# Kernel optimization log

Hardware: AMD Instinct MI355X
Metric: run time of the kernel (lower is better)

Reference implementation:

```python
import jax, jax.numpy as jnp
import numpy as np

NUM_HEADS = 8
EPS_OT = 0.05    # self.eps
BETA_T = 1.0     # self.beta_t
N_ITERS = 100    # Sinkhorn max_iter (reference runs all iterations; torch breaks early on convergence)


def setup_inputs() -> dict:
    key = jax.random.key(0)
    ks = jax.random.split(key, 10)
    B, N1, N2 = 16, 256, 576
    dim_t, dim_v, dim_out = 512, 512, 512
    s = 0.02  # conv1d k=1 init scale (stand-in for torch default init)
    f32 = jnp.float32
    return {
        "F_t": jax.random.normal(ks[0], (B, N1, dim_t), f32),
        "F_s": jax.random.normal(ks[1], (B, N2, dim_v), f32),
        # Conv1d(kernel_size=1) weights, squeezed to [out, in]; biases default-on in nn.Conv1d
        "Wq": jax.random.normal(ks[2], (dim_out, dim_t), f32) * s,
        "bq": jnp.zeros((dim_out,), f32),
        "Wk": jax.random.normal(ks[3], (dim_out, dim_v), f32) * s,
        "bk": jnp.zeros((dim_out,), f32),
        "Wv": jax.random.normal(ks[4], (dim_out, dim_v), f32) * s,
        "bv": jnp.zeros((dim_out,), f32),
        "Wp": jax.random.normal(ks[5], (dim_out, dim_out), f32) * s,
        "bp": jnp.zeros((dim_out,), f32),
    }


def sinkhorn_log_exp_sum(C, log_mu, log_nu, eps):
    # C: [BH, N1, N2]; fixed-length log-domain Sinkhorn.
    BH, N1, N2 = C.shape
    u0 = jnp.zeros((BH, N1), C.dtype)
    v0 = jnp.zeros((BH, N2), C.dtype)

    def body(carry, _):
        u, v = carry
        # single K per iteration; both u and v updates use the OLD (u, v), matching torch code
        K = (-C + u[:, :, None] + v[:, None, :]) / eps
        u_new = eps * (log_mu - jax.scipy.special.logsumexp(K, axis=2)) + u
        v_new = eps * (log_nu - jax.scipy.special.logsumexp(K, axis=1)) + v
        return (u_new, v_new), None

    (u, v), _ = jax.lax.scan(jax.checkpoint(body), (u0, v0), None, length=N_ITERS)
    return jnp.exp((-C + u[:, :, None] + v[:, None, :]) / eps)


def _l2norm(x, eps=1e-12):
    return x / jnp.maximum(jnp.linalg.norm(x, axis=-1, keepdims=True), eps)


def reference(F_t, F_s, Wq, bq, Wk, bk, Wv, bv, Wp, bp):
    B, N1, _ = F_t.shape
    N2 = F_s.shape[1]
    H = NUM_HEADS
    dim_out = Wq.shape[0]
    hd = dim_out // H

    # Conv1d(kernel=1) == pointwise linear over channel dim
    q = (F_t @ Wq.T + bq).reshape(B, N1, H, hd)
    k = (F_s @ Wk.T + bk).reshape(B, N2, H, hd)
    v = (F_s @ Wv.T + bv).reshape(B, N2, H, hd)

    q = _l2norm(q)
    k = _l2norm(k)

    sim = jnp.einsum('bnkc,bmkc->bknm', q, k) * BETA_T  # [B,H,N1,N2]
    wdist = (1.0 - sim).reshape(B * H, N1, N2)
    sim_f = sim.reshape(B * H, N1, N2)

    log_mu = jnp.log(jnp.asarray(1.0 / N1 + 1e-8, sim.dtype))
    log_nu = jnp.log(jnp.asarray(1.0 / N2 + 1e-8, sim.dtype))
    T = sinkhorn_log_exp_sum(wdist, log_mu, log_nu, EPS_OT)

    score_map = (N1 * N2 * sim_f * T).reshape(B, H, N1, N2)  # attn_drop = identity (p=0)
    F_t_a = jnp.einsum('bknm,bmkc->bnkc', score_map, v).reshape(B, N1, dim_out)
    F_t_a = F_t_a @ Wp.T + bp
    # torch: F_t_a / F_t_a.norm(dim=-1, keepdim=True)  (plain division, no eps clamp)
    F_t_a = F_t_a / jnp.linalg.norm(F_t_a, axis=-1, keepdims=True)
    return F_t_a  # proj_drop = identity (p=0)
```

## Files before the change

kernel.cpp:

```cpp
#include <hip/hip_runtime.h>
#include <math.h>

#define EPS_OT 0.05f
#define INV_EPS 20.0f

typedef unsigned short ushort_t;
typedef __attribute__((ext_vector_type(8))) short short8;
typedef __attribute__((ext_vector_type(4))) float f32x4;
union Pk { uint4 u; short8 s; };

__device__ __forceinline__ unsigned int f2bf(float f) {
  unsigned int u = __float_as_uint(f);
  return (u + 0x7FFFu + ((u >> 16) & 1u)) >> 16;
}
__device__ __forceinline__ float bf2f(unsigned int u) { return __uint_as_float(u << 16); }

__device__ __forceinline__ void bar_lds() {
  asm volatile("s_waitcnt lgkmcnt(0)" ::: "memory");
  __builtin_amdgcn_s_barrier();
  asm volatile("" ::: "memory");
}

__global__ __launch_bounds__(256) void pack_k(const float* __restrict__ F_t,
                                              const float* __restrict__ F_s,
                                              const float* __restrict__ Wq,
                                              const float* __restrict__ Wk,
                                              const float* __restrict__ Wv,
                                              const float* __restrict__ Wp,
                                              ushort_t* __restrict__ Fth, ushort_t* __restrict__ Ftl,
                                              ushort_t* __restrict__ Fsh, ushort_t* __restrict__ Fsl,
                                              ushort_t* __restrict__ Wqh, ushort_t* __restrict__ Wql,
                                              ushort_t* __restrict__ Wkh, ushort_t* __restrict__ Wkl,
                                              ushort_t* __restrict__ Wvh, ushort_t* __restrict__ Wvl,
                                              ushort_t* __restrict__ Wph) {
  const int blk = blockIdx.x;
  const float* src; ushort_t* dh; ushort_t* dl; size_t off;
  if (blk < 2048)      { src = F_t; dh = Fth; dl = Ftl; off = (size_t)blk * 1024; }
  else if (blk < 6656) { src = F_s; dh = Fsh; dl = Fsl; off = (size_t)(blk - 2048) * 1024; }
  else if (blk < 6912) { src = Wq;  dh = Wqh; dl = Wql; off = (size_t)(blk - 6656) * 1024; }
  else if (blk < 7168) { src = Wk;  dh = Wkh; dl = Wkl; off = (size_t)(blk - 6912) * 1024; }
  else if (blk < 7424) { src = Wv;  dh = Wvh; dl = Wvl; off = (size_t)(blk - 7168) * 1024; }
  else                 { src = Wp;  dh = Wph; dl = nullptr; off = (size_t)(blk - 7424) * 1024; }
  const size_t i = off + (size_t)threadIdx.x * 4;
  float4 f = *(const float4*)(src + i);
  unsigned int h0 = f2bf(f.x), h1 = f2bf(f.y), h2 = f2bf(f.z), h3 = f2bf(f.w);
  uint2 hh; hh.x = h0 | (h1 << 16); hh.y = h2 | (h3 << 16);
  *(uint2*)(dh + i) = hh;
  if (dl) {
    uint2 ll;
    ll.x = f2bf(f.x - bf2f(h0)) | (f2bf(f.y - bf2f(h1)) << 16);
    ll.y = f2bf(f.z - bf2f(h2)) | (f2bf(f.w - bf2f(h3)) << 16);
    *(uint2*)(dl + i) = ll;
  }
}

#define GEMM_HL_BODY()                                                                      \
  f32x4 acc[4] = {};                                                                        \
  for (int k0 = 0; k0 < 512; k0 += 64) {                                                    \
    uint4 a0 = *(const uint4*)(Xp_h + k0), a1 = *(const uint4*)(Xp_h + k0 + 8);             \
    uint4 b0 = *(const uint4*)(Xp_l + k0), b1 = *(const uint4*)(Xp_l + k0 + 8);             \
    uint4 c0 = *(const uint4*)(Wp_h + k0), c1 = *(const uint4*)(Wp_h + k0 + 8);             \
    uint4 d0 = *(const uint4*)(Wp_l + k0), d1 = *(const uint4*)(Wp_l + k0 + 8);             \
    __syncthreads();                                                                        \
    *(uint4*)&Xh[r][cg * 16] = a0; *(uint4*)&Xh[r][cg * 16 + 8] = a1;                       \
    *(uint4*)&Xl[r][cg * 16] = b0; *(uint4*)&Xl[r][cg * 16 + 8] = b1;                       \
    *(uint4*)&Wh[r][cg * 16] = c0; *(uint4*)&Wh[r][cg * 16 + 8] = c1;                       \
    *(uint4*)&Wl[r][cg * 16] = d0; *(uint4*)&Wl[r][cg * 16 + 8] = d1;                       \
    __syncthreads();                                                                        \
    _Pragma("unroll") for (int kst = 0; kst < 2; ++kst) {                                   \
      short8 ah = *(const short8*)&Xh[16 * w + li][kst * 32 + 8 * lg];                      \
      short8 al = *(const short8*)&Xl[16 * w + li][kst * 32 + 8 * lg];                      \
      _Pragma("unroll") for (int nt = 0; nt < 4; ++nt) {                                    \
        short8 bh = *(const short8*)&Wh[nt * 16 + li][kst * 32 + 8 * lg];                   \
        short8 bl = *(const short8*)&Wl[nt * 16 + li][kst * 32 + 8 * lg];                   \
        acc[nt] = __builtin_amdgcn_mfma_f32_16x16x32_bf16(ah, bh, acc[nt], 0, 0, 0);        \
        acc[nt] = __builtin_amdgcn_mfma_f32_16x16x32_bf16(ah, bl, acc[nt], 0, 0, 0);        \
        acc[nt] = __builtin_amdgcn_mfma_f32_16x16x32_bf16(al, bh, acc[nt], 0, 0, 0);        \
      }                                                                                     \
    }                                                                                       \
  }

#define GEMM_PL_BODY()                                                                      \
  f32x4 acc[4] = {};                                                                        \
  for (int k0 = 0; k0 < 512; k0 += 64) {                                                    \
    uint4 a0 = *(const uint4*)(Xp_h + k0), a1 = *(const uint4*)(Xp_h + k0 + 8);             \
    uint4 c0 = *(const uint4*)(Wp_h + k0), c1 = *(const uint4*)(Wp_h + k0 + 8);             \
    __syncthreads();                                                                        \
    *(uint4*)&Xh[r][cg * 16] = a0; *(uint4*)&Xh[r][cg * 16 + 8] = a1;                       \
    *(uint4*)&Wh[r][cg * 16] = c0; *(uint4*)&Wh[r][cg * 16 + 8] = c1;                       \
    __syncthreads();                                                                        \
    _Pragma("unroll") for (int kst = 0; kst < 2; ++kst) {                                   \
      short8 ah = *(const short8*)&Xh[16 * w + li][kst * 32 + 8 * lg];                      \
      _Pragma("unroll") for (int nt = 0; nt < 4; ++nt) {                                    \
        short8 bh = *(const short8*)&Wh[nt * 16 + li][kst * 32 + 8 * lg];                   \
        acc[nt] = __builtin_amdgcn_mfma_f32_16x16x32_bf16(ah, bh, acc[nt], 0, 0, 0);        \
      }                                                                                     \
    }                                                                                       \
  }

__global__ __launch_bounds__(256) void gemmnorm2_k(const ushort_t* __restrict__ Xg_h,
                                                   const ushort_t* __restrict__ Xg_l,
                                                   const ushort_t* __restrict__ Wg_h,
                                                   const ushort_t* __restrict__ Wg_l,
                                                   const float* __restrict__ bias,
                                                   ushort_t* __restrict__ oh,
                                                   ushort_t* __restrict__ ol, int Nn) {
  __shared__ ushort_t Xh[64][72], Xl[64][72], Wh[64][72], Wl[64][72];
  const int tid = threadIdx.x;
  const int w = tid >> 6, l = tid & 63, li = l & 15, lg = l >> 4;
  const int r = tid >> 2, cg = tid & 3;
  const int m0 = blockIdx.x << 6;
  const int h = blockIdx.y, n0 = h << 6;
  const ushort_t* Xp_h = Xg_h + (size_t)(m0 + r) * 512 + cg * 16;
  const ushort_t* Xp_l = Xg_l + (size_t)(m0 + r) * 512 + cg * 16;
  const ushort_t* Wp_h = Wg_h + (size_t)(n0 + r) * 512 + cg * 16;
  const ushort_t* Wp_l = Wg_l + (size_t)(n0 + r) * 512 + cg * 16;
  GEMM_HL_BODY()
  float v[4][4];
  float ss[4] = {0.f, 0.f, 0.f, 0.f};
#pragma unroll
  for (int nt = 0; nt < 4; ++nt) {
    float bb = bias[n0 + nt * 16 + li];
#pragma unroll
    for (int reg = 0; reg < 4; ++reg) {
      float y = acc[nt][reg] + bb;
      v[nt][reg] = y;
      ss[reg] = fmaf(y, y, ss[reg]);
    }
  }
#pragma unroll
  for (int off = 1; off < 16; off <<= 1)
#pragma unroll
    for (int reg = 0; reg < 4; ++reg) ss[reg] += __shfl_xor(ss[reg], off, 64);
  const int b = m0 / Nn;
  const int nbase = m0 - b * Nn;
  const size_t base = ((size_t)(b * 8 + h) * Nn + nbase + 16 * w + 4 * lg) * 64;
#pragma unroll
  for (int reg = 0; reg < 4; ++reg) {
    float inv = 1.0f / fmaxf(sqrtf(ss[reg]), 1e-12f);
#pragma unroll
    for (int nt = 0; nt < 4; ++nt) {
      float y = v[nt][reg] * inv;
      unsigned int hi = f2bf(y);
      size_t idx = base + (size_t)reg * 64 + nt * 16 + li;
      oh[idx] = (ushort_t)hi;
      ol[idx] = (ushort_t)f2bf(y - bf2f(hi));
    }
  }
}

__global__ __launch_bounds__(256) void gemmtrans2_k(const ushort_t* __restrict__ Xg_h,
                                                    const ushort_t* __restrict__ Wg_h,
                                                    const float* __restrict__ bias,
                                                    ushort_t* __restrict__ vt) {
  __shared__ ushort_t Xh[64][72], Wh[64][72];
  __shared__ ushort_t Vs[64 * 73];
  const int tid = threadIdx.x;
  const int w = tid >> 6, l = tid & 63, li = l & 15, lg = l >> 4;
  const int r = tid >> 2, cg = tid & 3;
  const int m0 = blockIdx.x << 6;
  const int h = blockIdx.y, n0 = h << 6;
  const ushort_t* Xp_h = Xg_h + (size_t)(m0 + r) * 512 + cg * 16;
  const ushort_t* Wp_h = Wg_h + (size_t)(n0 + r) * 512 + cg * 16;
  GEMM_PL_BODY()
#pragma unroll
  for (int nt = 0; nt < 4; ++nt) {
    float bb = bias[n0 + nt * 16 + li];
#pragma unroll
    for (int reg = 0; reg < 4; ++reg)
      Vs[(16 * w + 4 * lg + reg) * 73 + nt * 16 + li] = (ushort_t)f2bf(acc[nt][reg] + bb);
  }
  __syncthreads();
  const int a9 = m0 >> 6;
  const int b = a9 / 9;
  const int nbase = m0 - b * 576;
  const int s = b * 8 + h;
  const int c = tid >> 2, q4 = tid & 3;
  ushort_t tmp[16];
#pragma unroll
  for (int jj = 0; jj < 16; ++jj) tmp[jj] = Vs[(q4 * 16 + jj) * 73 + c];
  ushort_t* op = vt + ((size_t)s * 64 + c) * 576 + nbase + q4 * 16;
  *(uint4*)op = *(uint4*)&tmp[0];
  *(uint4*)(op + 8) = *(uint4*)&tmp[8];
}

__global__ __launch_bounds__(256) void gemmplain_k(const ushort_t* __restrict__ Xg_h,
                                                   const ushort_t* __restrict__ Wg_h,
                                                   const float* __restrict__ bias,
                                                   float* __restrict__ Y) {
  __shared__ ushort_t Xh[64][72], Wh[64][72];
  const int tid = threadIdx.x;
  const int w = tid >> 6, l = tid & 63, li = l & 15, lg = l >> 4;
  const int r = tid >> 2, cg = tid & 3;
  const int m0 = blockIdx.x << 6, n0 = blockIdx.y << 6;
  const ushort_t* Xp_h = Xg_h + (size_t)(m0 + r) * 512 + cg * 16;
  const ushort_t* Wp_h = Wg_h + (size_t)(n0 + r) * 512 + cg * 16;
  GEMM_PL_BODY()
#pragma unroll
  for (int nt = 0; nt < 4; ++nt) {
    float bb = bias[n0 + nt * 16 + li];
#pragma unroll
    for (int reg = 0; reg < 4; ++reg)
      Y[(size_t)(m0 + 16 * w + 4 * lg + reg) * 512 + n0 + nt * 16 + li] = acc[nt][reg] + bb;
  }
}

#define SK_SMEM 147456

__global__ __launch_bounds__(1024, 1) void sinkhorn17_k(const ushort_t* __restrict__ qh,
                                                        const ushort_t* __restrict__ ql,
                                                        const ushort_t* __restrict__ kh,
                                                        const ushort_t* __restrict__ kl,
                                                        ushort_t* __restrict__ Eo,
                                                        float* __restrict__ gA,
                                                        float* __restrict__ gB,
                                                        unsigned long long* __restrict__ gpart,
                                                        float C_mu, float C_nu) {
  extern __shared__ char smem[];
  const int g = blockIdx.x, s = g >> 1, rh = g & 1, pg = g ^ 1;
  const int tid = threadIdx.x, w = tid >> 6, l = tid & 63, li = l & 15, lg = l >> 4;
  unsigned long long* myP = gpart + (size_t)g * 1152;
  const unsigned long long* prP = gpart + (size_t)pg * 1152;

  ushort_t* Elds = (ushort_t*)smem;
  {
    const int rt = w & 7;
    const int qrow = rh * 128 + rt * 16 + li;
    const size_t qoff = ((size_t)s * 256 + qrow) * 64 + 8 * lg;
    short8 aH0 = *(const short8*)(qh + qoff), aH1 = *(const short8*)(qh + qoff + 32);
    short8 aL0 = *(const short8*)(ql + qoff), aL1 = *(const short8*)(ql + qoff + 32);
    const int c0 = (w >> 3) * 18;
    for (int ci = 0; ci < 18; ++ci) {
      const int ct = c0 + ci;
      const size_t koff = ((size_t)s * 576 + ct * 16 + li) * 64 + 8 * lg;
      short8 bH0 = *(const short8*)(kh + koff), bH1 = *(const short8*)(kh + koff + 32);
      short8 bL0 = *(const short8*)(kl + koff), bL1 = *(const short8*)(kl + koff + 32);
      f32x4 acc = {0.f, 0.f, 0.f, 0.f};
      acc = __builtin_amdgcn_mfma_f32_16x16x32_bf16(aH0, bH0, acc, 0, 0, 0);
      acc = __builtin_amdgcn_mfma_f32_16x16x32_bf16(aH1, bH1, acc, 0, 0, 0);
      acc = __builtin_amdgcn_mfma_f32_16x16x32_bf16(aH0, bL0, acc, 0, 0, 0);
      acc = __builtin_amdgcn_mfma_f32_16x16x32_bf16(aH1, bL1, acc, 0, 0, 0);
      acc = __builtin_amdgcn_mfma_f32_16x16x32_bf16(aL0, bH0, acc, 0, 0, 0);
      acc = __builtin_amdgcn_mfma_f32_16x16x32_bf16(aL1, bH1, acc, 0, 0, 0);
#pragma unroll
      for (int reg = 0; reg < 4; ++reg) {
        float e = __expf((acc[reg] - 1.0f) * INV_EPS);
        Elds[(rt * 16 + 4 * lg + reg) * 576 + ct * 16 + li] = (ushort_t)f2bf(e);
      }
    }
  }
  __syncthreads();
  {
    uint4* Eg4 = (uint4*)(Eo + (size_t)s * 147456 + (size_t)rh * 73728);
    const uint4* El4 = (const uint4*)Elds;
    for (int idx = tid; idx < 9216; idx += 1024) Eg4[idx] = El4[idx];
  }

  const int art = (w & 7) * 16 + li;
  const int akb = (w >> 3) * 9;
  short8 afr[9];
#pragma unroll
  for (int c = 0; c < 9; ++c)
    afr[c] = *(const short8*)(Elds + art * 576 + (akb + c) * 32 + 8 * lg);

  short8 bfr0, bfr1, bfr2, bfr3, bfr4, bfr5, bfr6, bfr7, bfr8, bfr9, bfr10, bfr11;
#define BFR_BUILD(dst, tc, q)                                                  \
  {                                                                            \
    const ushort_t* p = Elds + ((q) * 32 + 8 * lg) * 576 + (tc) * 16 + li;     \
    Pk pk;                                                                     \
    pk.u.x = (unsigned int)p[0]    | ((unsigned int)p[576]  << 16);            \
    pk.u.y = (unsigned int)p[1152] | ((unsigned int)p[1728] << 16);            \
    pk.u.z = (unsigned int)p[2304] | ((unsigned int)p[2880] << 16);            \
    pk.u.w = (unsigned int)p[3456] | ((unsigned int)p[4032] << 16);            \
    dst = pk.s;                                                                \
  }
  BFR_BUILD(bfr0, w, 0) BFR_BUILD(bfr1, w, 1) BFR_BUILD(bfr2, w, 2) BFR_BUILD(bfr3, w, 3)
  BFR_BUILD(bfr4, w + 16, 0) BFR_BUILD(bfr5, w + 16, 1)
  BFR_BUILD(bfr6, w + 16, 2) BFR_BUILD(bfr7, w + 16, 3)
  if (w < 4) {
    BFR_BUILD(bfr8, w + 32, 0) BFR_BUILD(bfr9, w + 32, 1)
    BFR_BUILD(bfr10, w + 32, 2) BFR_BUILD(bfr11, w + 32, 3)
  } else {
    bfr8 = bfr0; bfr9 = bfr1; bfr10 = bfr2; bfr11 = bfr3;
  }
  __syncthreads();

  float* uu = (float*)smem;
  float* vv = uu + 128;
  ushort_t* au = (ushort_t*)(vv + 576);
  ushort_t* bv = au + 128;
  float* rpart = (float*)(au + 768);
  float* cso = rpart + 256;

  if (tid < 128) { uu[tid] = 0.0f; au[tid] = (ushort_t)0x3F80; }
  if (tid < 576) { vv[tid] = 0.0f; bv[tid] = (ushort_t)0x3F80; }
  __syncthreads();

  const int jj = tid - 128;
  const bool poller = (tid >= 128) && (tid < 704);

  for (int t = 0; t < 100; ++t) {
    const int par = t & 1;
    {
      Pk q0, q1, q2, q3;
      q0.u = *(const uint4*)(au + 8 * lg);
      q1.u = *(const uint4*)(au + 32 + 8 * lg);
      q2.u = *(const uint4*)(au + 64 + 8 * lg);
      q3.u = *(const uint4*)(au + 96 + 8 * lg);
#define MV2_TILE(tc, f0, f1, f2, f3)                                                  \
      {                                                                               \
        f32x4 a2 = {0.f, 0.f, 0.f, 0.f}, b2 = {0.f, 0.f, 0.f, 0.f};                   \
        a2 = __builtin_amdgcn_mfma_f32_16x16x32_bf16(q0.s, f0, a2, 0, 0, 0);          \
        b2 = __builtin_amdgcn_mfma_f32_16x16x32_bf16(q2.s, f2, b2, 0, 0, 0);          \
        a2 = __builtin_amdgcn_mfma_f32_16x16x32_bf16(q1.s, f1, a2, 0, 0, 0);          \
        b2 = __builtin_amdgcn_mfma_f32_16x16x32_bf16(q3.s, f3, b2, 0, 0, 0);          \
        if (l < 16) {                                                                 \
          const int col = (tc) * 16 + l;                                              \
          float cs = a2[0] + b2[0];                                                   \
          cso[col] = cs;                                                              \
          unsigned long long pv = (unsigned long long)__float_as_uint(cs) |           \
                                  ((unsigned long long)(unsigned int)(t + 1) << 32);  \
          __hip_atomic_store(&myP[par * 576 + col], pv, __ATOMIC_RELAXED,             \
                             __HIP_MEMORY_SCOPE_AGENT);                               \
        }                                                                             \
      }
      MV2_TILE(w, bfr0, bfr1, bfr2, bfr3)
      MV2_TILE(w + 16, bfr4, bfr5, bfr6, bfr7)
      if (w < 4) MV2_TILE(w + 32, bfr8, bfr9, bfr10, bfr11)
    }
    {
      f32x4 x1 = {0.f, 0.f, 0.f, 0.f}, y1 = {0.f, 0.f, 0.f, 0.f}, z1 = {0.f, 0.f, 0.f, 0.f};
      Pk b0, b1, b2, b3, b4, b5, b6, b7, b8;
      b0.u = *(const uint4*)(bv + (akb + 0) * 32 + 8 * lg);
      b1.u = *(const uint4*)(bv + (akb + 1) * 32 + 8 * lg);
      b2.u = *(const uint4*)(bv + (akb + 2) * 32 + 8 * lg);
      b3.u = *(const uint4*)(bv + (akb + 3) * 32 + 8 * lg);
      b4.u = *(const uint4*)(bv + (akb + 4) * 32 + 8 * lg);
      b5.u = *(const uint4*)(bv + (akb + 5) * 32 + 8 * lg);
      b6.u = *(const uint4*)(bv + (akb + 6) * 32 + 8 * lg);
      b7.u = *(const uint4*)(bv + (akb + 7) * 32 + 8 * lg);
      b8.u = *(const uint4*)(bv + (akb + 8) * 32 + 8 * lg);
      x1 = __builtin_amdgcn_mfma_f32_16x16x32_bf16(b0.s, afr[0], x1, 0, 0, 0);
      y1 = __builtin_amdgcn_mfma_f32_16x16x32_bf16(b3.s, afr[3], y1, 0, 0, 0);
      z1 = __builtin_amdgcn_mfma_f32_16x16x32_bf16(b6.s, afr[6], z1, 0, 0, 0);
      x1 = __builtin_amdgcn_mfma_f32_16x16x32_bf16(b1.s, afr[1], x1, 0, 0, 0);
      y1 = __builtin_amdgcn_mfma_f32_16x16x32_bf16(b4.s, afr[4], y1, 0, 0, 0);
      z1 = __builtin_amdgcn_mfma_f32_16x16x32_bf16(b7.s, afr[7], z1, 0, 0, 0);
      x1 = __builtin_amdgcn_mfma_f32_16x16x32_bf16(b2.s, afr[2], x1, 0, 0, 0);
      y1 = __builtin_amdgcn_mfma_f32_16x16x32_bf16(b5.s, afr[5], y1, 0, 0, 0);
      z1 = __builtin_amdgcn_mfma_f32_16x16x32_bf16(b8.s, afr[8], z1, 0, 0, 0);
      if (l < 16) rpart[(w >> 3) * 128 + (w & 7) * 16 + l] = (x1[0] + y1[0]) + z1[0];
    }
    __builtin_amdgcn_sched_barrier(0);
    unsigned long long p0 = 0;
    if (poller)
      p0 = __hip_atomic_load(&prP[par * 576 + jj], __ATOMIC_RELAXED, __HIP_MEMORY_SCOPE_AGENT);
    bar_lds();
    if (tid < 128) {
      float rs = rpart[tid] + rpart[128 + tid];
      float un = C_mu - EPS_OT * __logf(rs);
      uu[tid] = un;
      au[tid] = (ushort_t)f2bf(__expf(fminf(fmaxf(un * INV_EPS, -80.f), 80.f)));
    } else if (tid < 704) {
      const unsigned int tg = (unsigned int)(t + 1);
      while ((unsigned int)(p0 >> 32) != tg) {
        __builtin_amdgcn_s_sleep(1);
        p0 = __hip_atomic_load(&prP[par * 576 + jj], __ATOMIC_RELAXED, __HIP_MEMORY_SCOPE_AGENT);
      }
      float tot = cso[jj] + __uint_as_float((unsigned int)p0);
      float vn = C_nu - EPS_OT * __logf(tot);
      vv[jj] = vn;
      bv[jj] = (ushort_t)f2bf(__expf(fminf(fmaxf(vn * INV_EPS, -80.f), 80.f)));
    }
    bar_lds();
  }
  if (rh == 0 && tid >= 128 && tid < 704) {
    unsigned long long p0;
    for (;;) {
      p0 = __hip_atomic_load(&prP[576 + jj], __ATOMIC_RELAXED, __HIP_MEMORY_SCOPE_AGENT);
      if ((unsigned int)(p0 >> 32) == 100u) break;
      __builtin_amdgcn_s_sleep(1);
    }
    float tot = cso[jj] + __uint_as_float((unsigned int)p0);
    vv[jj] = C_nu - EPS_OT * __logf(tot);
  }
  __syncthreads();
  if (tid < 128) gA[(size_t)s * 256 + rh * 128 + tid] = uu[tid] * INV_EPS;
  if (rh == 0 && tid < 576) gB[(size_t)s * 576 + tid] = vv[tid] * INV_EPS + 11.9012851f;
}

__global__ __launch_bounds__(256) void scorev2_k(const ushort_t* __restrict__ E,
                                                 const ushort_t* __restrict__ vt,
                                                 const float* __restrict__ gA,
                                                 const float* __restrict__ gB,
                                                 ushort_t* __restrict__ Y) {
  __shared__ float gBs[576];
  const int s = blockIdx.x, i0 = blockIdx.y << 6;
  const int tid = threadIdx.x;
  const int w = tid >> 6, l = tid & 63, li = l & 15, lg = l >> 4;
  for (int j = tid; j < 576; j += 256) gBs[j] = gB[(size_t)s * 576 + j];
  const float ga = gA[(size_t)s * 256 + i0 + 16 * w + li];
  const ushort_t* Erow = E + (size_t)s * 147456 + (size_t)(i0 + 16 * w + li) * 576;
  f32x4 acc[4] = {};
  __syncthreads();
  for (int kst = 0; kst < 18; ++kst) {
    const int jb = kst * 32 + 8 * lg;
    Pk eu; eu.u = *(const uint4*)(Erow + jb);
    float pv[8];
#pragma unroll
    for (int jj = 0; jj < 8; ++jj) {
      unsigned int us = (unsigned int)(unsigned short)eu.s[jj];
      float e = bf2f(us);
      float le = __logf(e);
      pv[jj] = (1.0f + EPS_OT * le) * __expf(le + ga + gBs[jb + jj]);
    }
    Pk ph, pl;
#pragma unroll
    for (int jj = 0; jj < 8; ++jj) {
      unsigned int h = f2bf(pv[jj]);
      ((unsigned short*)&ph.s)[jj] = (unsigned short)h;
      ((unsigned short*)&pl.s)[jj] = (unsigned short)f2bf(pv[jj] - bf2f(h));
    }
#pragma unroll
    for (int nt = 0; nt < 4; ++nt) {
      Pk vf; vf.u = *(const uint4*)(vt + ((size_t)s * 64 + nt * 16 + li) * 576 + jb);
      acc[nt] = __builtin_amdgcn_mfma_f32_16x16x32_bf16(ph.s, vf.s, acc[nt], 0, 0, 0);
      acc[nt] = __builtin_amdgcn_mfma_f32_16x16x32_bf16(pl.s, vf.s, acc[nt], 0, 0, 0);
    }
  }
  const int b = s >> 3, h = s & 7;
#pragma unroll
  for (int nt = 0; nt < 4; ++nt)
#pragma unroll
    for (int reg = 0; reg < 4; ++reg)
      Y[((size_t)(b * 256 + i0 + 16 * w + 4 * lg + reg) << 9) + (h << 6) + nt * 16 + li] =
          (ushort_t)f2bf(acc[nt][reg]);
}

__global__ __launch_bounds__(256) void rownorm_k(const float* __restrict__ X,
                                                 float* __restrict__ out) {
  const size_t row = blockIdx.x;
  const int tid = threadIdx.x;
  float x0 = X[(row << 9) + tid], x1 = X[(row << 9) + 256 + tid];
  float st = fmaf(x0, x0, x1 * x1);
#pragma unroll
  for (int off = 32; off; off >>= 1) st += __shfl_xor(st, off, 64);
  __shared__ float ps[4];
  if ((tid & 63) == 0) ps[tid >> 6] = st;
  __syncthreads();
  const float inv = 1.0f / sqrtf(ps[0] + ps[1] + ps[2] + ps[3]);
  out[(row << 9) + tid] = x0 * inv;
  out[(row << 9) + 256 + tid] = x1 * inv;
}

extern "C" void kernel_launch(void* const* d_in, const int* in_sizes, int n_in,
                              void* d_out, int out_size, void* d_ws, size_t ws_size,
                              hipStream_t stream) {
  const float* F_t = (const float*)d_in[0];
  const float* F_s = (const float*)d_in[1];
  const float* Wq = (const float*)d_in[2];
  const float* bq = (const float*)d_in[3];
  const float* Wk = (const float*)d_in[4];
  const float* bk = (const float*)d_in[5];
  const float* Wv = (const float*)d_in[6];
  const float* bvb = (const float*)d_in[7];
  const float* Wp = (const float*)d_in[8];
  const float* bp = (const float*)d_in[9];
  float* out = (float*)d_out;

  ushort_t* u0 = (ushort_t*)d_ws;
  ushort_t* Fth = u0;
  ushort_t* Ftl = Fth + 2097152;
  ushort_t* Fsh = Ftl + 2097152;
  ushort_t* Fsl = Fsh + 4718592;
  ushort_t* Wqh = Fsl + 4718592;
  ushort_t* Wql = Wqh + 262144;
  ushort_t* Wkh = Wql + 262144;
  ushort_t* Wkl = Wkh + 262144;
  ushort_t* Wvh = Wkl + 262144;
  ushort_t* Wvl = Wvh + 262144;
  ushort_t* Wph = Wvl + 262144;
  ushort_t* qh = Wph + 262144;
  ushort_t* ql = qh + 2097152;
  ushort_t* kh = ql + 2097152;
  ushort_t* kl = kh + 4718592;
  ushort_t* vt = kl + 4718592;
  ushort_t* Eb = vt + 4718592;
  ushort_t* T0b = Eb + 18874368;
  float* T1 = (float*)(T0b + 2097152);
  float* gA = T1 + 2097152;
  float* gB = gA + 32768;
  unsigned long long* gpart = (unsigned long long*)(gB + 73728);

  const float C_mu = (float)(0.05 * log(1.0 / 256.0 + 1e-8));
  const float C_nu = (float)(0.05 * log(1.0 / 576.0 + 1e-8));

  (void)hipFuncSetAttribute((const void*)sinkhorn17_k,
                            hipFuncAttributeMaxDynamicSharedMemorySize, SK_SMEM);

  pack_k<<<7680, 256, 0, stream>>>(F_t, F_s, Wq, Wk, Wv, Wp, Fth, Ftl, Fsh, Fsl,
                                   Wqh, Wql, Wkh, Wkl, Wvh, Wvl, Wph);
  gemmnorm2_k<<<dim3(64, 8), 256, 0, stream>>>(Fth, Ftl, Wqh, Wql, bq, qh, ql, 256);
  gemmnorm2_k<<<dim3(144, 8), 256, 0, stream>>>(Fsh, Fsl, Wkh, Wkl, bk, kh, kl, 576);
  gemmtrans2_k<<<dim3(144, 8), 256, 0, stream>>>(Fsh, Wvh, bvb, vt);
  sinkhorn17_k<<<256, 1024, SK_SMEM, stream>>>(qh, ql, kh, kl, Eb, gA, gB, gpart, C_mu, C_nu);
  scorev2_k<<<dim3(128, 4), 256, 0, stream>>>(Eb, vt, gA, gB, T0b);
  gemmplain_k<<<dim3(64, 8), 256, 0, stream>>>(T0b, Wph, bp, T1);
  rownorm_k<<<4096, 256, 0, stream>>>(T1, out);
}
```

Before: 359.3 us.

## Fuse score-times-V epilogue into Sinkhorn kernel using LDS-resident E

Folds the score/V product into the Sinkhorn kernel's epilogue. E now stays in shared memory (the u/v scratch moves past it), so the global write of E, the gA/gB writes and the separate scorev2 launch that re-read E are all removed. Each block computes its own 128 rows of output, with 16 waves each covering two 16-column tiles. The risk is that this MFMA phase runs on only 256 blocks. The final v update after the last iteration is also no longer exchanged with the partner block, which may change numerics.

```diff
diff --git a/kernel.cpp b/kernel.cpp
--- a/kernel.cpp
+++ b/kernel.cpp
@@ -205,15 +205,14 @@
   }
 }
 
-#define SK_SMEM 147456
-
-__global__ __launch_bounds__(1024, 1) void sinkhorn17_k(const ushort_t* __restrict__ qh,
+#define SK_SMEM 155136
+
+__global__ __launch_bounds__(1024, 1) void sinkhorn18_k(const ushort_t* __restrict__ qh,
                                                         const ushort_t* __restrict__ ql,
                                                         const ushort_t* __restrict__ kh,
                                                         const ushort_t* __restrict__ kl,
-                                                        ushort_t* __restrict__ Eo,
-                                                        float* __restrict__ gA,
-                                                        float* __restrict__ gB,
+                                                        const ushort_t* __restrict__ vt,
+                                                        ushort_t* __restrict__ Y,
                                                         unsigned long long* __restrict__ gpart,
                                                         float C_mu, float C_nu) {
   extern __shared__ char smem[];
@@ -250,11 +249,6 @@
     }
   }
   __syncthreads();
-  {
-    uint4* Eg4 = (uint4*)(Eo + (size_t)s * 147456 + (size_t)rh * 73728);
-    const uint4* El4 = (const uint4*)Elds;
-    for (int idx = tid; idx < 9216; idx += 1024) Eg4[idx] = El4[idx];
-  }
 
   const int art = (w & 7) * 16 + li;
   const int akb = (w >> 3) * 9;
@@ -283,9 +277,8 @@
   } else {
     bfr8 = bfr0; bfr9 = bfr1; bfr10 = bfr2; bfr11 = bfr3;
   }
-  __syncthreads();
-
-  float* uu = (float*)smem;
+
+  float* uu = (float*)(smem + 147456);
   float* vv = uu + 128;
   ushort_t* au = (ushort_t*)(vv + 576);
   ushort_t* bv = au + 128;
@@ -374,67 +367,50 @@
     }
     bar_lds();
   }
-  if (rh == 0 && tid >= 128 && tid < 704) {
-    unsigned long long p0;
-    for (;;) {
-      p0 = __hip_atomic_load(&prP[576 + jj], __ATOMIC_RELAXED, __HIP_MEMORY_SCOPE_AGENT);
-      if ((unsigned int)(p0 >> 32) == 100u) break;
-      __builtin_amdgcn_s_sleep(1);
-    }
-    float tot = cso[jj] + __uint_as_float((unsigned int)p0);
-    vv[jj] = C_nu - EPS_OT * __logf(tot);
-  }
-  __syncthreads();
-  if (tid < 128) gA[(size_t)s * 256 + rh * 128 + tid] = uu[tid] * INV_EPS;
-  if (rh == 0 && tid < 576) gB[(size_t)s * 576 + tid] = vv[tid] * INV_EPS + 11.9012851f;
-}
-
-__global__ __launch_bounds__(256) void scorev2_k(const ushort_t* __restrict__ E,
-                                                 const ushort_t* __restrict__ vt,
-                                                 const float* __restrict__ gA,
-                                                 const float* __restrict__ gB,
-                                                 ushort_t* __restrict__ Y) {
-  __shared__ float gBs[576];
-  const int s = blockIdx.x, i0 = blockIdx.y << 6;
-  const int tid = threadIdx.x;
-  const int w = tid >> 6, l = tid & 63, li = l & 15, lg = l >> 4;
-  for (int j = tid; j < 576; j += 256) gBs[j] = gB[(size_t)s * 576 + j];
-  const float ga = gA[(size_t)s * 256 + i0 + 16 * w + li];
-  const ushort_t* Erow = E + (size_t)s * 147456 + (size_t)(i0 + 16 * w + li) * 576;
-  f32x4 acc[4] = {};
-  __syncthreads();
-  for (int kst = 0; kst < 18; ++kst) {
-    const int jb = kst * 32 + 8 * lg;
-    Pk eu; eu.u = *(const uint4*)(Erow + jb);
-    float pv[8];
-#pragma unroll
-    for (int jj = 0; jj < 8; ++jj) {
-      unsigned int us = (unsigned int)(unsigned short)eu.s[jj];
-      float e = bf2f(us);
-      float le = __logf(e);
-      pv[jj] = (1.0f + EPS_OT * le) * __expf(le + ga + gBs[jb + jj]);
-    }
-    Pk ph, pl;
-#pragma unroll
-    for (int jj = 0; jj < 8; ++jj) {
-      unsigned int h = f2bf(pv[jj]);
-      ((unsigned short*)&ph.s)[jj] = (unsigned short)h;
-      ((unsigned short*)&pl.s)[jj] = (unsigned short)f2bf(pv[jj] - bf2f(h));
-    }
-#pragma unroll
-    for (int nt = 0; nt < 4; ++nt) {
-      Pk vf; vf.u = *(const uint4*)(vt + ((size_t)s * 64 + nt * 16 + li) * 576 + jb);
-      acc[nt] = __builtin_amdgcn_mfma_f32_16x16x32_bf16(ph.s, vf.s, acc[nt], 0, 0, 0);
-      acc[nt] = __builtin_amdgcn_mfma_f32_16x16x32_bf16(pl.s, vf.s, acc[nt], 0, 0, 0);
-    }
-  }
-  const int b = s >> 3, h = s & 7;
-#pragma unroll
-  for (int nt = 0; nt < 4; ++nt)
-#pragma unroll
-    for (int reg = 0; reg < 4; ++reg)
-      Y[((size_t)(b * 256 + i0 + 16 * w + 4 * lg + reg) << 9) + (h << 6) + nt * 16 + li] =
-          (ushort_t)f2bf(acc[nt][reg]);
+
+  if (tid < 576) cso[tid] = vv[tid] * INV_EPS + 11.9012851f;
+  bar_lds();
+
+  {
+    const int rt = w & 7;
+    const int ntb2 = (w >> 3) << 1;
+    const float ga = uu[rt * 16 + li] * INV_EPS;
+    const ushort_t* Erow = Elds + (size_t)(rt * 16 + li) * 576;
+    f32x4 acc0 = {0.f, 0.f, 0.f, 0.f}, acc1 = {0.f, 0.f, 0.f, 0.f};
+    for (int kst = 0; kst < 18; ++kst) {
+      const int jb = kst * 32 + 8 * lg;
+      Pk eu; eu.u = *(const uint4*)(Erow + jb);
+      float pv[8];
+#pragma unroll
+      for (int j2 = 0; j2 < 8; ++j2) {
+        unsigned int us = (unsigned int)(unsigned short)eu.s[j2];
+        float e = bf2f(us);
+        float le = __logf(e);
+        pv[j2] = (1.0f + EPS_OT * le) * __expf(le + ga + cso[jb + j2]);
+      }
+      Pk ph, pl;
+#pragma unroll
+      for (int j2 = 0; j2 < 8; ++j2) {
+        unsigned int hv = f2bf(pv[j2]);
+        ((unsigned short*)&ph.s)[j2] = (unsigned short)hv;
+        ((unsigned short*)&pl.s)[j2] = (unsigned short)f2bf(pv[j2] - bf2f(hv));
+      }
+      Pk vf0, vf1;
+      vf0.u = *(const uint4*)(vt + ((size_t)s * 64 + (ntb2 + 0) * 16 + li) * 576 + jb);
+      vf1.u = *(const uint4*)(vt + ((size_t)s * 64 + (ntb2 + 1) * 16 + li) * 576 + jb);
+      acc0 = __builtin_amdgcn_mfma_f32_16x16x32_bf16(ph.s, vf0.s, acc0, 0, 0, 0);
+      acc0 = __builtin_amdgcn_mfma_f32_16x16x32_bf16(pl.s, vf0.s, acc0, 0, 0, 0);
+      acc1 = __builtin_amdgcn_mfma_f32_16x16x32_bf16(ph.s, vf1.s, acc1, 0, 0, 0);
+      acc1 = __builtin_amdgcn_mfma_f32_16x16x32_bf16(pl.s, vf1.s, acc1, 0, 0, 0);
+    }
+    const int b = s >> 3, h = s & 7;
+    const int grow = b * 256 + rh * 128 + rt * 16 + 4 * lg;
+#pragma unroll
+    for (int reg = 0; reg < 4; ++reg) {
+      Y[((size_t)(grow + reg) << 9) + (h << 6) + (ntb2 + 0) * 16 + li] = (ushort_t)f2bf(acc0[reg]);
+      Y[((size_t)(grow + reg) << 9) + (h << 6) + (ntb2 + 1) * 16 + li] = (ushort_t)f2bf(acc1[reg]);
+    }
+  }
 }
 
 __global__ __launch_bounds__(256) void rownorm_k(const float* __restrict__ X,
@@ -495,7 +471,7 @@
   const float C_mu = (float)(0.05 * log(1.0 / 256.0 + 1e-8));
   const float C_nu = (float)(0.05 * log(1.0 / 576.0 + 1e-8));
 
-  (void)hipFuncSetAttribute((const void*)sinkhorn17_k,
+  (void)hipFuncSetAttribute((const void*)sinkhorn18_k,
                             hipFuncAttributeMaxDynamicSharedMemorySize, SK_SMEM);
 
   pack_k<<<7680, 256, 0, stream>>>(F_t, F_s, Wq, Wk, Wv, Wp, Fth, Ftl, Fsh, Fsl,
@@ -503,8 +479,7 @@
   gemmnorm2_k<<<dim3(64, 8), 256, 0, stream>>>(Fth, Ftl, Wqh, Wql, bq, qh, ql, 256);
   gemmnorm2_k<<<dim3(144, 8), 256, 0, stream>>>(Fsh, Fsl, Wkh, Wkl, bk, kh, kl, 576);
   gemmtrans2_k<<<dim3(144, 8), 256, 0, stream>>>(Fsh, Wvh, bvb, vt);
-  sinkhorn17_k<<<256, 1024, SK_SMEM, stream>>>(qh, ql, kh, kl, Eb, gA, gB, gpart, C_mu, C_nu);
-  scorev2_k<<<dim3(128, 4), 256, 0, stream>>>(Eb, vt, gA, gB, T0b);
+  sinkhorn18_k<<<256, 1024, SK_SMEM, stream>>>(qh, ql, kh, kl, vt, T0b, gpart, C_mu, C_nu);
   gemmplain_k<<<dim3(64, 8), 256, 0, stream>>>(T0b, Wph, bp, T1);
   rownorm_k<<<4096, 256, 0, stream>>>(T1, out);
 }
```

New measurement: 418.4 us. 1.16x slower.
